# Optimization experiments

Measured on AMD Instinct MI355X. Metric: run time of the kernel, lower is better.

The kernel has to match this reference:

```python
import jax, jax.numpy as jnp
import numpy as np

TAU = 2.0        # LIF membrane time constant
VTH = 1.0        # spike threshold
VRESET = 0.0     # hard reset voltage
ALPHA = 2.0      # ATan surrogate alpha
LN_EPS = 1e-5


@jax.custom_vjp
def atan_spike(x):
    # Heaviside forward, ATan surrogate backward (spikingjelly surrogate.ATan)
    return (x >= 0.0).astype(x.dtype)

def _atan_fwd(x):
    return atan_spike(x), x

def _atan_bwd(x, g):
    z = (jnp.pi / 2.0) * ALPHA * x
    return (g * (ALPHA / 2.0) / (1.0 + z * z),)

atan_spike.defvjp(_atan_fwd, _atan_bwd)


def layer_norm(x, w, b):
    mu = jnp.mean(x, axis=-1, keepdims=True)
    var = jnp.mean(jnp.square(x - mu), axis=-1, keepdims=True)
    return (x - mu) * jax.lax.rsqrt(var + LN_EPS) * w + b


def time_shift(x):
    # x: [B,T,C] -> x shifted by one step in time, zero-padded at t=0
    return jnp.pad(x, ((0, 0), (1, 0), (0, 0)))[:, :-1]


def wkv(time_decay, time_first, k, v):
    # Numerically-stable RWKV WKV recurrence. k, v: [B,T,C]
    w = -jnp.exp(time_decay)  # [C]
    u = time_first            # [C]
    B, T, C = k.shape
    kT = jnp.moveaxis(k, 1, 0)  # [T,B,C]
    vT = jnp.moveaxis(v, 1, 0)
    init = (jnp.zeros((B, C), k.dtype),
            jnp.zeros((B, C), k.dtype),
            jnp.full((B, C), -1e38, k.dtype))

    def step(carry, kv_t):
        aa, bb, pp = carry
        kt, vt = kv_t
        ww = u + kt
        p = jnp.maximum(pp, ww)
        e1 = jnp.exp(pp - p)
        e2 = jnp.exp(ww - p)
        y = (e1 * aa + e2 * vt) / (e1 * bb + e2)
        ww2 = pp + w
        p2 = jnp.maximum(ww2, kt)
        e1b = jnp.exp(ww2 - p2)
        e2b = jnp.exp(kt - p2)
        return (e1b * aa + e2b * vt, e1b * bb + e2b, p2), y

    _, yT = jax.lax.scan(step, init, (kT, vT))
    return jnp.moveaxis(yT, 0, 1)  # [B,T,C]


def lif(x):
    # MultiStepLIFNode: tau=2, decay_input=True, v_th=1, hard reset to 0.
    # Recurrence runs over the sequence dim (permute(1,0,2) in torch is layout only).
    xT = jnp.moveaxis(x, 1, 0)  # [T,B,C]
    v0 = jnp.zeros_like(xT[0])

    def step(v, xt):
        v = v + (xt - (v - VRESET)) / TAU
        s = atan_spike(v - VTH)
        v = (1.0 - s) * v + s * VRESET
        return v, s

    _, sT = jax.lax.scan(step, v0, xT)
    return jnp.moveaxis(sT, 0, 1)


def rwkv_time_mix(x, time_decay, time_first, mix_k, mix_v, mix_r, Wk, Wv, Wr, Wo):
    xx = time_shift(x)
    xk = x * mix_k + xx * (1.0 - mix_k)
    xv = x * mix_v + xx * (1.0 - mix_v)
    xr = x * mix_r + xx * (1.0 - mix_r)
    k = jnp.einsum('btc,cd->btd', xk, Wk)
    v = jnp.einsum('btc,cd->btd', xv, Wv)
    r = jax.nn.sigmoid(jnp.einsum('btc,cd->btd', xr, Wr))
    y = wkv(time_decay, time_first, k, v)
    return jnp.einsum('btc,cd->btd', r * y, Wo)


def rwkv_channel_mix(x, mix_k, mix_r, Wk, Wv, Wr):
    xx = time_shift(x)
    xk = x * mix_k + xx * (1.0 - mix_k)
    xr = x * mix_r + xx * (1.0 - mix_r)
    k = jnp.square(jax.nn.relu(jnp.einsum('btc,ch->bth', xk, Wk)))  # relu^2
    kv = jnp.einsum('bth,hc->btc', k, Wv)
    return jax.nn.sigmoid(jnp.einsum('btc,cd->btd', xr, Wr)) * kv


def setup_inputs() -> dict:
    key = jax.random.key(0)
    B, T, C, H = 8, 2048, 768, 3072
    ks = jax.random.split(key, 20)
    p = lambda k, shape, s=0.02: (jax.random.normal(k, shape, jnp.float32) * s)
    u = lambda k, shape: jax.random.uniform(k, shape, jnp.float32)
    return {
        'x': jax.random.normal(ks[0], (B, T, C), jnp.float32),
        'ln1_w': jnp.ones((C,), jnp.float32), 'ln1_b': jnp.zeros((C,), jnp.float32),
        'ln2_w': jnp.ones((C,), jnp.float32), 'ln2_b': jnp.zeros((C,), jnp.float32),
        'att_time_decay': p(ks[1], (C,), 1.0),
        'att_time_first': p(ks[2], (C,), 1.0),
        'att_mix_k': u(ks[3], (C,)), 'att_mix_v': u(ks[4], (C,)), 'att_mix_r': u(ks[5], (C,)),
        'att_Wk': p(ks[6], (C, C)), 'att_Wv': p(ks[7], (C, C)),
        'att_Wr': p(ks[8], (C, C)), 'att_Wo': p(ks[9], (C, C)),
        'ffn_mix_k': u(ks[10], (C,)), 'ffn_mix_r': u(ks[11], (C,)),
        'ffn_Wk': p(ks[12], (C, H)), 'ffn_Wv': p(ks[13], (H, C)), 'ffn_Wr': p(ks[14], (C, C)),
    }


def reference(x, ln1_w, ln1_b, ln2_w, ln2_b,
              att_time_decay, att_time_first, att_mix_k, att_mix_v, att_mix_r,
              att_Wk, att_Wv, att_Wr, att_Wo,
              ffn_mix_k, ffn_mix_r, ffn_Wk, ffn_Wv, ffn_Wr):
    # Block.forward with layer_id != 0 (no ln0, att path); dropout in eval mode.
    a = rwkv_time_mix(layer_norm(x, ln1_w, ln1_b), att_time_decay, att_time_first,
                      att_mix_k, att_mix_v, att_mix_r, att_Wk, att_Wv, att_Wr, att_Wo)
    x = x + lif(a)
    f = rwkv_channel_mix(layer_norm(x, ln2_w, ln2_b), ffn_mix_k, ffn_mix_r,
                         ffn_Wk, ffn_Wv, ffn_Wr)
    x = x + lif(f)
    return x
```

## Files before the change

kernel.cpp:

```cpp
#include <hip/hip_runtime.h>

#define B_ 8
#define T_ 2048
#define C_ 768
#define H_ 3072
#define BT_ (B_ * T_)
#define BC_ (B_ * C_)
#define WSEG 128
#define NWSEG 16
#define LSEG 128
#define NLSEG 16
#define LWARM 96

typedef unsigned short u16;
typedef short bf16x8 __attribute__((ext_vector_type(8)));
typedef float f32x4 __attribute__((ext_vector_type(4)));

__device__ __forceinline__ float b2f(u16 u) {
    union { unsigned i; float f; } w; w.i = ((unsigned)u) << 16; return w.f;
}
__device__ __forceinline__ u16 f2b(float f) {
    union { float f; unsigned i; } w; w.f = f;
    return (u16)((w.i + 0x7fffu + ((w.i >> 16) & 1u)) >> 16);
}

typedef __attribute__((address_space(3))) unsigned int lds_u32;
typedef const __attribute__((address_space(1))) unsigned int glb_u32;
__device__ __forceinline__ void gld_lds16(const void* g, void* l) {
    __builtin_amdgcn_global_load_lds((glb_u32*)g, (lds_u32*)l, 16, 0, 0);
}

template<int NOUT>
__global__ void lnmix(const float* __restrict__ x, const float* __restrict__ w,
                      const float* __restrict__ b,
                      const float* __restrict__ m1, const float* __restrict__ m2,
                      const float* __restrict__ m3,
                      u16* __restrict__ o1, u16* __restrict__ o2, u16* __restrict__ o3) {
    int row = blockIdx.x;
    int t = row % T_;
    const float* xr = x + (size_t)row * C_;
    const float* xp = xr - C_;
    int tid = threadIdx.x;
    float s = 0.f, s2 = 0.f, ps = 0.f, ps2 = 0.f;
    for (int i = tid; i < C_; i += 256) {
        float v = xr[i]; s += v; s2 += v * v;
        if (t > 0) { float u = xp[i]; ps += u; ps2 += u * u; }
    }
    for (int off = 32; off > 0; off >>= 1) {
        s += __shfl_down(s, off);  s2 += __shfl_down(s2, off);
        ps += __shfl_down(ps, off); ps2 += __shfl_down(ps2, off);
    }
    __shared__ float red[4][4];
    int wid = tid >> 6, lane = tid & 63;
    if (lane == 0) { red[wid][0] = s; red[wid][1] = s2; red[wid][2] = ps; red[wid][3] = ps2; }
    __syncthreads();
    if (tid == 0) {
        float a0 = 0, a1 = 0, a2 = 0, a3 = 0;
        for (int i = 0; i < 4; ++i) { a0 += red[i][0]; a1 += red[i][1]; a2 += red[i][2]; a3 += red[i][3]; }
        red[0][0] = a0; red[0][1] = a1; red[0][2] = a2; red[0][3] = a3;
    }
    __syncthreads();
    float mu = red[0][0] * (1.f / C_);
    float rs = rsqrtf(red[0][1] * (1.f / C_) - mu * mu + 1e-5f);
    float pmu = red[0][2] * (1.f / C_);
    float prs = rsqrtf(red[0][3] * (1.f / C_) - pmu * pmu + 1e-5f);
    size_t ob = (size_t)row * C_;
    for (int i = tid; i < C_; i += 256) {
        float wi = w[i], bi = b[i];
        float n = (xr[i] - mu) * rs * wi + bi;
        float np = (t > 0) ? (xp[i] - pmu) * prs * wi + bi : 0.f;
        o1[ob + i] = f2b(fmaf(m1[i], n - np, np));
        o2[ob + i] = f2b(fmaf(m2[i], n - np, np));
        if constexpr (NOUT == 3) o3[ob + i] = f2b(fmaf(m3[i], n - np, np));
    }
}

struct TCJ { const float* s; u16* d; int R, Ncol, nbx, b0; };
struct TC7 { TCJ j[7]; };
__global__ void tcast_all(TC7 jobs) {
    __shared__ float t[32][33];
    int bid = blockIdx.x;
    int ji = 0;
#pragma unroll
    for (int k = 1; k < 7; ++k) if (bid >= jobs.j[k].b0) ji = k;
    TCJ jb = jobs.j[ji];
    int local = bid - jb.b0;
    int bx = local % jb.nbx, by = local / jb.nbx;
    int c0 = bx * 32, r0 = by * 32;
    int col = threadIdx.x & 31, rw = threadIdx.x >> 5;
#pragma unroll
    for (int i = 0; i < 4; ++i) {
        int r = rw + i * 8;
        t[r][col] = jb.s[(size_t)(r0 + r) * jb.Ncol + c0 + col];
    }
    __syncthreads();
#pragma unroll
    for (int i = 0; i < 4; ++i) {
        int r = rw + i * 8;
        jb.d[(size_t)(c0 + r) * jb.R + r0 + col] = f2b(t[col][r]);
    }
}

__device__ __forceinline__ void gemm_core256(const u16* __restrict__ A,
                                             const u16* __restrict__ WT,
                                             int K, int m0, int n0,
                                             u16* L, f32x4 acc[8][4]) {
    const int tid = threadIdx.x;
    const int lane = tid & 63, wid = tid >> 6;
    const int wr = wid >> 2, wc = wid & 3;
    const int r16 = lane & 15, g = lane >> 4;

    const int srow = tid >> 2;
    const int sunit = tid & 3;
    const int sx = (srow >> 1) & 3;
    const u16* gA0 = A + (size_t)(m0 + srow) * K + ((sunit ^ sx) << 3);
    const u16* gA1 = gA0 + (size_t)128 * K;
    const u16* gB0 = WT + (size_t)(n0 + srow) * K + ((sunit ^ sx) << 3);
    const u16* gB1 = gB0 + (size_t)128 * K;
    u16* lA0 = L + tid * 8;
    u16* lA1 = L + 4096 + tid * 8;
    u16* lB0 = L + 8192 + tid * 8;
    u16* lB1 = L + 12288 + tid * 8;

    int offA[8], offB[4];
#pragma unroll
    for (int m = 0; m < 8; ++m) {
        int row = wr * 128 + m * 16 + r16;
        offA[m] = row * 32 + (g ^ ((row >> 1) & 3)) * 8;
    }
#pragma unroll
    for (int n = 0; n < 4; ++n) {
        int rob = wc * 64 + n * 16 + r16;
        offB[n] = 8192 + rob * 32 + (g ^ ((rob >> 1) & 3)) * 8;
    }

#define STGA(buf) do { \
        gld_lds16(gA0, lA0 + (buf) * 16384); gld_lds16(gA1, lA1 + (buf) * 16384); \
        gA0 += 32; gA1 += 32; } while (0)
#define STGB(buf) do { \
        gld_lds16(gB0, lB0 + (buf) * 16384); gld_lds16(gB1, lB1 + (buf) * 16384); \
        gB0 += 32; gB1 += 32; } while (0)

    const int nt = K >> 5;
    STGA(0); STGB(0);
    STGA(1); STGB(1);
    asm volatile("s_waitcnt vmcnt(4)" ::: "memory");
    __builtin_amdgcn_sched_barrier(0);
    __builtin_amdgcn_s_barrier();

    int rb = 0, wb = 2;
    for (int t = 0; t < nt; ++t) {
        const u16* Lb = L + rb * 16384;
        const bool stg = (t + 2 < nt);
        bf16x8 a0[4], bg[4];
#pragma unroll
        for (int m = 0; m < 4; ++m) a0[m] = *(const bf16x8*)(Lb + offA[m]);
#pragma unroll
        for (int n = 0; n < 4; ++n) bg[n] = *(const bf16x8*)(Lb + offB[n]);
        __builtin_amdgcn_sched_barrier(0);
        if (stg) STGA(wb);
        __builtin_amdgcn_s_barrier();
        asm volatile("s_waitcnt lgkmcnt(0)" ::: "memory");
        __builtin_amdgcn_sched_barrier(0);
        __builtin_amdgcn_s_setprio(1);
#pragma unroll
        for (int m = 0; m < 4; ++m)
#pragma unroll
            for (int n = 0; n < 4; ++n)
                acc[m][n] = __builtin_amdgcn_mfma_f32_16x16x32_bf16(a0[m], bg[n], acc[m][n], 0, 0, 0);
        __builtin_amdgcn_s_setprio(0);
        __builtin_amdgcn_sched_barrier(0);
        __builtin_amdgcn_s_barrier();
        bf16x8 a1[4];
#pragma unroll
        for (int m = 0; m < 4; ++m) a1[m] = *(const bf16x8*)(Lb + offA[4 + m]);
        __builtin_amdgcn_sched_barrier(0);
        if (stg) STGB(wb);
        __builtin_amdgcn_s_barrier();
        asm volatile("s_waitcnt lgkmcnt(0)" ::: "memory");
        __builtin_amdgcn_sched_barrier(0);
        __builtin_amdgcn_s_setprio(1);
#pragma unroll
        for (int m = 0; m < 4; ++m)
#pragma unroll
            for (int n = 0; n < 4; ++n)
                acc[4 + m][n] = __builtin_amdgcn_mfma_f32_16x16x32_bf16(a1[m], bg[n], acc[4 + m][n], 0, 0, 0);
        __builtin_amdgcn_s_setprio(0);
        __builtin_amdgcn_sched_barrier(0);
        if (t + 1 < nt) {
            if (stg) asm volatile("s_waitcnt vmcnt(4)" ::: "memory");
            else     asm volatile("s_waitcnt vmcnt(0)" ::: "memory");
            __builtin_amdgcn_sched_barrier(0);
            __builtin_amdgcn_s_barrier();
        }
        rb = (rb == 2) ? 0 : rb + 1;
        wb = (wb == 2) ? 0 : wb + 1;
    }
#undef STGA
#undef STGB
}

__device__ __forceinline__ void xcd_remap2(int& bx, int& by) {
    const int gx = gridDim.x;
    const int nwg = gx * gridDim.y;
    const int lin = blockIdx.y * gx + blockIdx.x;
    const int q = nwg >> 3, r = nwg & 7;
    const int xcd = lin & 7, pos = lin >> 3;
    const int nid = (xcd < r ? xcd * (q + 1) : r * (q + 1) + (xcd - r) * q) + pos;
    bx = nid % gx;
    by = nid / gx;
}

__device__ __forceinline__ void epilogue256(f32x4 acc[8][4], u16* O, const u16* Emul,
                                            int m0, int n0, int N, int mode, bool emul) {
    const int lane = threadIdx.x & 63, wid = threadIdx.x >> 6;
    const int wr = wid >> 2, wc = wid & 3;
    const int r16 = lane & 15, g = lane >> 4;
#pragma unroll
    for (int m = 0; m < 8; ++m)
#pragma unroll
        for (int n = 0; n < 4; ++n)
#pragma unroll
            for (int j = 0; j < 4; ++j) {
                int row = m0 + wr * 128 + m * 16 + g * 4 + j;
                int col = n0 + wc * 64 + n * 16 + r16;
                float v = acc[m][n][j];
                if (mode == 1) v = 1.f / (1.f + expf(-v));
                else if (mode == 2) { v = fmaxf(v, 0.f); v = v * v; }
                size_t o = (size_t)row * N + col;
                if (emul) v *= b2f(Emul[o]);
                O[o] = f2b(v);
            }
}

template<int MODE, bool EMUL>
__global__ __launch_bounds__(512, 1)
void gemm256(const u16* __restrict__ A, const u16* __restrict__ WT,
             u16* __restrict__ Cout, const u16* __restrict__ Emul, int N, int K) {
    __shared__ u16 L[49152];
    int bx, by;
    xcd_remap2(bx, by);
    const int m0 = by << 8, n0 = bx << 8;
    f32x4 acc[8][4];
#pragma unroll
    for (int i = 0; i < 8; ++i)
#pragma unroll
        for (int j = 0; j < 4; ++j)
#pragma unroll
            for (int q = 0; q < 4; ++q) acc[i][j][q] = 0.f;
    gemm_core256(A, WT, K, m0, n0, L, acc);
    epilogue256(acc, Cout, Emul, m0, n0, N, MODE, EMUL);
}

struct P3 {
    const u16 *A0, *A1, *A2;
    const u16 *W0, *W1, *W2;
    u16 *O0, *O1, *O2;
};
__global__ __launch_bounds__(512, 1)
void proj3(P3 p, int N, int K) {
    __shared__ u16 L[49152];
    const int z = blockIdx.z;
    const u16* A = (z == 0) ? p.A0 : (z == 1) ? p.A1 : p.A2;
    const u16* W = (z == 0) ? p.W0 : (z == 1) ? p.W1 : p.W2;
    u16* O = (z == 0) ? p.O0 : (z == 1) ? p.O1 : p.O2;
    int bx, by;
    xcd_remap2(bx, by);
    const int m0 = by << 8, n0 = bx << 8;
    f32x4 acc[8][4];
#pragma unroll
    for (int i = 0; i < 8; ++i)
#pragma unroll
        for (int j = 0; j < 4; ++j)
#pragma unroll
            for (int q = 0; q < 4; ++q) acc[i][j][q] = 0.f;
    gemm_core256(A, W, K, m0, n0, L, acc);
    epilogue256(acc, O, nullptr, m0, n0, N, (z == 2) ? 1 : 0, false);
}

struct J2 {
    const u16 *A0, *W0; u16 *O0;
    const u16 *A1, *W1; u16 *O1;
};
__global__ __launch_bounds__(512, 1)
void ffn1rr(J2 p, int K) {
    __shared__ u16 L[49152];
    int bx, by;
    xcd_remap2(bx, by);
    const bool isF = (bx < 12);
    const u16* A = isF ? p.A0 : p.A1;
    const u16* W = isF ? p.W0 : p.W1;
    u16* O = isF ? p.O0 : p.O1;
    const int N = isF ? 3072 : 768;
    const int m0 = by << 8;
    const int n0 = (isF ? bx : bx - 12) << 8;
    f32x4 acc[8][4];
#pragma unroll
    for (int i = 0; i < 8; ++i)
#pragma unroll
        for (int j = 0; j < 4; ++j)
#pragma unroll
            for (int q = 0; q < 4; ++q) acc[i][j][q] = 0.f;
    gemm_core256(A, W, K, m0, n0, L, acc);
    epilogue256(acc, O, nullptr, m0, n0, N, isF ? 2 : 1, false);
}

__global__ void wkv_p1(const float* __restrict__ td, const u16* __restrict__ K,
                       const u16* __restrict__ V, float* __restrict__ st) {
    int bc = blockIdx.x * 256 + threadIdx.x;
    int seg = blockIdx.y;
    int b = bc / C_, c = bc - b * C_;
    float w = -expf(td[c]);
    size_t off = (size_t)b * T_ * C_ + (size_t)seg * WSEG * C_ + c;
    float aa = 0.f, bb = 0.f, pp = -1e38f;
#pragma unroll 4
    for (int i = 0; i < WSEG; ++i) {
        float kt = b2f(K[off + (size_t)i * C_]);
        float vt = b2f(V[off + (size_t)i * C_]);
        float ww2 = pp + w;
        float p2 = fmaxf(ww2, kt);
        float e1 = expf(ww2 - p2);
        float e2 = expf(kt - p2);
        aa = e1 * aa + e2 * vt;
        bb = e1 * bb + e2;
        pp = p2;
    }
    int sidx = seg * 3 * BC_ + bc;
    st[sidx] = aa; st[sidx + BC_] = bb; st[sidx + 2 * BC_] = pp;
}

__global__ void wkv_p2(const float* __restrict__ td, const float* __restrict__ st,
                       float* __restrict__ ini) {
    int bc = blockIdx.x * 256 + threadIdx.x;
    int c = bc % C_;
    float wL = -expf(td[c]) * (float)WSEG;
    float aa = 0.f, bb = 0.f, pp = -1e38f;
    for (int s = 0; s < NWSEG; ++s) {
        int sidx = s * 3 * BC_ + bc;
        ini[sidx] = aa; ini[sidx + BC_] = bb; ini[sidx + 2 * BC_] = pp;
        float la = st[sidx], lb = st[sidx + BC_], lp = st[sidx + 2 * BC_];
        float ppw = pp + wL;
        float p = fmaxf(ppw, lp);
        float e1 = expf(ppw - p), e2 = expf(lp - p);
        aa = e1 * aa + e2 * la;
        bb = e1 * bb + e2 * lb;
        pp = p;
    }
}

__global__ void wkv_p3(const float* __restrict__ td, const float* __restrict__ tf,
                       const u16* __restrict__ K, const u16* __restrict__ V,
                       const u16* __restrict__ R, const float* __restrict__ ini,
                       u16* __restrict__ RY) {
    int bc = blockIdx.x * 256 + threadIdx.x;
    int seg = blockIdx.y;
    int b = bc / C_, c = bc - b * C_;
    float w = -expf(td[c]);
    float u = tf[c];
    int sidx = seg * 3 * BC_ + bc;
    float aa = ini[sidx], bb = ini[sidx + BC_], pp = ini[sidx + 2 * BC_];
    size_t off = (size_t)b * T_ * C_ + (size_t)seg * WSEG * C_ + c;
#pragma unroll 4
    for (int i = 0; i < WSEG; ++i) {
        float kt = b2f(K[off + (size_t)i * C_]);
        float vt = b2f(V[off + (size_t)i * C_]);
        float rr = b2f(R[off + (size_t)i * C_]);
        float ww = u + kt;
        float p = fmaxf(pp, ww);
        float e1 = expf(pp - p);
        float e2 = expf(ww - p);
        RY[off + (size_t)i * C_] = f2b(rr * (e1 * aa + e2 * vt) / (e1 * bb + e2));
        float ww2 = pp + w;
        float p2 = fmaxf(ww2, kt);
        float e1b = expf(ww2 - p2);
        float e2b = expf(kt - p2);
        aa = e1b * aa + e2b * vt;
        bb = e1b * bb + e2b;
        pp = p2;
    }
}

__global__ void lif_add_b(const u16* __restrict__ cur, const float* __restrict__ base,
                          float* __restrict__ out) {
    int bc = blockIdx.x * 256 + threadIdx.x;
    int seg = blockIdx.y;
    int b = bc / C_, c = bc - b * C_;
    size_t rowbase = (size_t)b * T_ * C_ + c;
    int t0 = seg * LSEG;
    int tw = t0 - LWARM; if (tw < 0) tw = 0;
    int nw = t0 - tw;
    float v = 0.f;
    const u16* cp = cur + rowbase + (size_t)tw * C_;
#pragma unroll 8
    for (int i = 0; i < nw; ++i) {
        float xt = b2f(cp[(size_t)i * C_]);
        v += (xt - v) * 0.5f;
        v = (v >= 1.f) ? 0.f : v;
    }
    const u16* c2 = cur + rowbase + (size_t)t0 * C_;
    const float* bp = base + rowbase + (size_t)t0 * C_;
    float* op = out + rowbase + (size_t)t0 * C_;
#pragma unroll 8
    for (int i = 0; i < LSEG; ++i) {
        float xt = b2f(c2[(size_t)i * C_]);
        v += (xt - v) * 0.5f;
        float sp = (v >= 1.f) ? 1.f : 0.f;
        op[(size_t)i * C_] = bp[(size_t)i * C_] + sp;
        v = (sp > 0.f) ? 0.f : v;
    }
}

extern "C" void kernel_launch(void* const* d_in, const int* in_sizes, int n_in,
                              void* d_out, int out_size, void* d_ws, size_t ws_size,
                              hipStream_t stream) {
    const float* x    = (const float*)d_in[0];
    const float* ln1w = (const float*)d_in[1];
    const float* ln1b = (const float*)d_in[2];
    const float* ln2w = (const float*)d_in[3];
    const float* ln2b = (const float*)d_in[4];
    const float* td   = (const float*)d_in[5];
    const float* tf   = (const float*)d_in[6];
    const float* amk  = (const float*)d_in[7];
    const float* amv  = (const float*)d_in[8];
    const float* amr  = (const float*)d_in[9];
    const float* aWk  = (const float*)d_in[10];
    const float* aWv  = (const float*)d_in[11];
    const float* aWr  = (const float*)d_in[12];
    const float* aWo  = (const float*)d_in[13];
    const float* fmk  = (const float*)d_in[14];
    const float* fmr  = (const float*)d_in[15];
    const float* fWk  = (const float*)d_in[16];
    const float* fWv  = (const float*)d_in[17];
    const float* fWr  = (const float*)d_in[18];
    float* out = (float*)d_out;

    const size_t NBC = (size_t)BT_ * C_;
    u16* WkT = (u16*)d_ws;
    u16* WvT = WkT + 589824;
    u16* WrT = WvT + 589824;
    u16* WoT = WrT + 589824;
    u16* FrT = WoT + 589824;
    u16* FkT = FrT + 589824;
    u16* FvT = FkT + 2359296;
    float* st  = (float*)(FvT + 2359296);
    float* ini = st + NWSEG * 3 * BC_;
    u16* S0 = (u16*)(ini + NWSEG * 3 * BC_);
    u16* S1 = S0 + NBC;
    u16* S2 = S1 + NBC;
    u16* S3 = S2 + NBC;
    u16* Hbuf = S3 + NBC;
    size_t fixed_b = (size_t)((char*)Hbuf - (char*)d_ws);

    int NCH = 4;
    if (ws_size >= fixed_b + ((size_t)BT_ * H_ + NBC) * 2) NCH = 1;
    else if (ws_size >= fixed_b + ((size_t)(BT_ / 2) * H_ + NBC / 2) * 2) NCH = 2;
    const int CH = BT_ / NCH;
    u16* Fbuf = Hbuf + (size_t)CH * H_;

    u16* Kb = (u16*)d_out;
    u16* Vb = Kb + NBC;

    {
        TC7 jobs;
        const float* srcs[7] = {aWk, aWv, aWr, aWo, fWr, fWk, fWv};
        u16* dsts[7] = {WkT, WvT, WrT, WoT, FrT, FkT, FvT};
        int Rs[7]    = {768, 768, 768, 768, 768, 768, 3072};
        int Ns[7]    = {768, 768, 768, 768, 768, 3072, 768};
        int b0 = 0;
        for (int k = 0; k < 7; ++k) {
            jobs.j[k].s = srcs[k]; jobs.j[k].d = dsts[k];
            jobs.j[k].R = Rs[k]; jobs.j[k].Ncol = Ns[k];
            jobs.j[k].nbx = Ns[k] / 32; jobs.j[k].b0 = b0;
            b0 += (Ns[k] / 32) * (Rs[k] / 32);
        }
        tcast_all<<<b0, 256, 0, stream>>>(jobs);
    }

    lnmix<3><<<BT_, 256, 0, stream>>>(x, ln1w, ln1b, amk, amv, amr, S0, S1, S2);
    {
        P3 p{S0, S1, S2, WkT, WvT, WrT, Kb, Vb, S3};
        proj3<<<dim3(3, 64, 3), 512, 0, stream>>>(p, C_, C_);
    }
    wkv_p1<<<dim3(BC_ / 256, NWSEG), 256, 0, stream>>>(td, Kb, Vb, st);
    wkv_p2<<<BC_ / 256, 256, 0, stream>>>(td, st, ini);
    wkv_p3<<<dim3(BC_ / 256, NWSEG), 256, 0, stream>>>(td, tf, Kb, Vb, S3, ini, S0);
    gemm256<0, false><<<dim3(3, 64), 512, 0, stream>>>(S0, WoT, S1, nullptr, C_, C_);
    lif_add_b<<<dim3(BC_ / 256, NLSEG), 256, 0, stream>>>(S1, x, out);
    lnmix<2><<<BT_, 256, 0, stream>>>(out, ln2w, ln2b, fmk, fmr, nullptr, S0, S1, nullptr);

    if (NCH == 1) {
        J2 p{S0, FkT, Hbuf, S1, FrT, S2};
        ffn1rr<<<dim3(15, 64), 512, 0, stream>>>(p, C_);
        gemm256<0, true><<<dim3(3, 64), 512, 0, stream>>>(Hbuf, FvT, Fbuf, S2, C_, H_);
        lif_add_b<<<dim3(BC_ / 256, NLSEG), 256, 0, stream>>>(Fbuf, out, out);
    } else {
        gemm256<1, false><<<dim3(3, 64), 512, 0, stream>>>(S1, FrT, S2, nullptr, C_, C_);
        for (int ch = 0; ch < NCH; ++ch) {
            const u16* xk2c = S0 + (size_t)ch * CH * C_;
            const u16* rrc  = S2 + (size_t)ch * CH * C_;
            gemm256<2, false><<<dim3(12, CH / 256), 512, 0, stream>>>(xk2c, FkT, Hbuf, nullptr, H_, C_);
            gemm256<0, true><<<dim3(3, CH / 256), 512, 0, stream>>>(Hbuf, FvT, Fbuf, rrc, C_, H_);
            lif_add_b<<<dim3((CH / T_) * C_ / 256, NLSEG), 256, 0, stream>>>(
                Fbuf, out + (size_t)ch * CH * C_, out + (size_t)ch * CH * C_);
        }
    }
}
```

Measured before the change: 597.3 us.

## Switch GEMM core to BK=64 double-buffered LDS pipeline with fewer barriers

Restructures the shared GEMM core from a triple-buffered BK=32 pipeline to a double-buffered BK=64 pipeline, using a new 8-way XOR swizzle for 64-wide rows. Each iteration loads all A and B fragments for two K-halves and issues 64 MFMAs between barriers, cutting barriers and loop overhead per K step. LDS use grows to 128 KB per block. Prefetch depth drops to one tile, and each step waits on vmcnt(0), which may expose global-load latency.

Measured after the change: 571.1 us. 4.4% less time.

```diff
diff --git a/kernel.cpp b/kernel.cpp
--- a/kernel.cpp
+++ b/kernel.cpp
@@ -110,91 +110,85 @@
     const int wr = wid >> 2, wc = wid & 3;
     const int r16 = lane & 15, g = lane >> 4;
 
-    const int srow = tid >> 2;
-    const int sunit = tid & 3;
-    const int sx = (srow >> 1) & 3;
-    const u16* gA0 = A + (size_t)(m0 + srow) * K + ((sunit ^ sx) << 3);
-    const u16* gA1 = gA0 + (size_t)128 * K;
-    const u16* gB0 = WT + (size_t)(n0 + srow) * K + ((sunit ^ sx) << 3);
-    const u16* gB1 = gB0 + (size_t)128 * K;
-    u16* lA0 = L + tid * 8;
-    u16* lA1 = L + 4096 + tid * 8;
-    u16* lB0 = L + 8192 + tid * 8;
-    u16* lB1 = L + 12288 + tid * 8;
+    const int srow = tid >> 3;
+    const int sunit = tid & 7;
+    const int ssw = sunit ^ (srow & 7);
+    const u16* gA = A + (size_t)(m0 + srow) * K + ssw * 8;
+    const u16* gB = WT + (size_t)(n0 + srow) * K + ssw * 8;
+    u16* lA = L + tid * 8;
+    u16* lB = L + 16384 + tid * 8;
+
+#define STGA(buf) do { \
+        gld_lds16(gA,                   lA + (buf) * 32768); \
+        gld_lds16(gA + (size_t)64 * K,  lA + (buf) * 32768 + 4096); \
+        gld_lds16(gA + (size_t)128 * K, lA + (buf) * 32768 + 8192); \
+        gld_lds16(gA + (size_t)192 * K, lA + (buf) * 32768 + 12288); \
+        gA += 64; } while (0)
+#define STGB(buf) do { \
+        gld_lds16(gB,                   lB + (buf) * 32768); \
+        gld_lds16(gB + (size_t)64 * K,  lB + (buf) * 32768 + 4096); \
+        gld_lds16(gB + (size_t)128 * K, lB + (buf) * 32768 + 8192); \
+        gld_lds16(gB + (size_t)192 * K, lB + (buf) * 32768 + 12288); \
+        gB += 64; } while (0)
 
     int offA[8], offB[4];
 #pragma unroll
     for (int m = 0; m < 8; ++m) {
         int row = wr * 128 + m * 16 + r16;
-        offA[m] = row * 32 + (g ^ ((row >> 1) & 3)) * 8;
+        offA[m] = row * 64 + (g ^ (row & 7)) * 8;
     }
 #pragma unroll
     for (int n = 0; n < 4; ++n) {
         int rob = wc * 64 + n * 16 + r16;
-        offB[n] = 8192 + rob * 32 + (g ^ ((rob >> 1) & 3)) * 8;
-    }
-
-#define STGA(buf) do { \
-        gld_lds16(gA0, lA0 + (buf) * 16384); gld_lds16(gA1, lA1 + (buf) * 16384); \
-        gA0 += 32; gA1 += 32; } while (0)
-#define STGB(buf) do { \
-        gld_lds16(gB0, lB0 + (buf) * 16384); gld_lds16(gB1, lB1 + (buf) * 16384); \
-        gB0 += 32; gB1 += 32; } while (0)
-
-    const int nt = K >> 5;
+        offB[n] = 16384 + rob * 64 + (g ^ (rob & 7)) * 8;
+    }
+
+    const int nt = K >> 6;
     STGA(0); STGB(0);
-    STGA(1); STGB(1);
-    asm volatile("s_waitcnt vmcnt(4)" ::: "memory");
+    asm volatile("s_waitcnt vmcnt(0)" ::: "memory");
     __builtin_amdgcn_sched_barrier(0);
     __builtin_amdgcn_s_barrier();
 
-    int rb = 0, wb = 2;
     for (int t = 0; t < nt; ++t) {
-        const u16* Lb = L + rb * 16384;
-        const bool stg = (t + 2 < nt);
-        bf16x8 a0[4], bg[4];
-#pragma unroll
-        for (int m = 0; m < 4; ++m) a0[m] = *(const bf16x8*)(Lb + offA[m]);
-#pragma unroll
-        for (int n = 0; n < 4; ++n) bg[n] = *(const bf16x8*)(Lb + offB[n]);
+        const u16* Lb = L + (t & 1) * 32768;
+        const bool stg = (t + 1 < nt);
+        bf16x8 a0[8], b0[4];
+#pragma unroll
+        for (int m = 0; m < 8; ++m) a0[m] = *(const bf16x8*)(Lb + offA[m]);
+#pragma unroll
+        for (int n = 0; n < 4; ++n) b0[n] = *(const bf16x8*)(Lb + offB[n]);
         __builtin_amdgcn_sched_barrier(0);
-        if (stg) STGA(wb);
-        __builtin_amdgcn_s_barrier();
+        if (stg) { STGA((t + 1) & 1); STGB((t + 1) & 1); }
         asm volatile("s_waitcnt lgkmcnt(0)" ::: "memory");
         __builtin_amdgcn_sched_barrier(0);
         __builtin_amdgcn_s_setprio(1);
 #pragma unroll
-        for (int m = 0; m < 4; ++m)
+        for (int m = 0; m < 8; ++m)
 #pragma unroll
             for (int n = 0; n < 4; ++n)
-                acc[m][n] = __builtin_amdgcn_mfma_f32_16x16x32_bf16(a0[m], bg[n], acc[m][n], 0, 0, 0);
+                acc[m][n] = __builtin_amdgcn_mfma_f32_16x16x32_bf16(a0[m], b0[n], acc[m][n], 0, 0, 0);
         __builtin_amdgcn_s_setprio(0);
         __builtin_amdgcn_sched_barrier(0);
-        __builtin_amdgcn_s_barrier();
-        bf16x8 a1[4];
-#pragma unroll
-        for (int m = 0; m < 4; ++m) a1[m] = *(const bf16x8*)(Lb + offA[4 + m]);
-        __builtin_amdgcn_sched_barrier(0);
-        if (stg) STGB(wb);
-        __builtin_amdgcn_s_barrier();
+        bf16x8 a1[8], b1[4];
+#pragma unroll
+        for (int m = 0; m < 8; ++m) a1[m] = *(const bf16x8*)(Lb + (offA[m] ^ 32));
+#pragma unroll
+        for (int n = 0; n < 4; ++n) b1[n] = *(const bf16x8*)(Lb + (offB[n] ^ 32));
         asm volatile("s_waitcnt lgkmcnt(0)" ::: "memory");
         __builtin_amdgcn_sched_barrier(0);
         __builtin_amdgcn_s_setprio(1);
 #pragma unroll
-        for (int m = 0; m < 4; ++m)
+        for (int m = 0; m < 8; ++m)
 #pragma unroll
             for (int n = 0; n < 4; ++n)
-                acc[4 + m][n] = __builtin_amdgcn_mfma_f32_16x16x32_bf16(a1[m], bg[n], acc[4 + m][n], 0, 0, 0);
+                acc[m][n] = __builtin_amdgcn_mfma_f32_16x16x32_bf16(a1[m], b1[n], acc[m][n], 0, 0, 0);
         __builtin_amdgcn_s_setprio(0);
         __builtin_amdgcn_sched_barrier(0);
-        if (t + 1 < nt) {
-            if (stg) asm volatile("s_waitcnt vmcnt(4)" ::: "memory");
-            else     asm volatile("s_waitcnt vmcnt(0)" ::: "memory");
+        if (stg) {
+            asm volatile("s_waitcnt vmcnt(0)" ::: "memory");
             __builtin_amdgcn_sched_barrier(0);
             __builtin_amdgcn_s_barrier();
         }
-        rb = (rb == 2) ? 0 : rb + 1;
-        wb = (wb == 2) ? 0 : wb + 1;
     }
 #undef STGA
 #undef STGB
@@ -237,7 +231,7 @@
 __global__ __launch_bounds__(512, 1)
 void gemm256(const u16* __restrict__ A, const u16* __restrict__ WT,
              u16* __restrict__ Cout, const u16* __restrict__ Emul, int N, int K) {
-    __shared__ u16 L[49152];
+    __shared__ u16 L[65536];
     int bx, by;
     xcd_remap2(bx, by);
     const int m0 = by << 8, n0 = bx << 8;
@@ -259,7 +253,7 @@
 };
 __global__ __launch_bounds__(512, 1)
 void proj3(P3 p, int N, int K) {
-    __shared__ u16 L[49152];
+    __shared__ u16 L[65536];
     const int z = blockIdx.z;
     const u16* A = (z == 0) ? p.A0 : (z == 1) ? p.A1 : p.A2;
     const u16* W = (z == 0) ? p.W0 : (z == 1) ? p.W1 : p.W2;
@@ -284,7 +278,7 @@
 };
 __global__ __launch_bounds__(512, 1)
 void ffn1rr(J2 p, int K) {
-    __shared__ u16 L[49152];
+    __shared__ u16 L[65536];
     int bx, by;
     xcd_remap2(bx, by);
     const bool isF = (bx < 12);
```
